# Kernel tuning notes

Measured on AMD Instinct MI355X. Metric: run time of the kernel, lower is better.

The kernel has to match this reference:

```python
import jax, jax.numpy as jnp
import numpy as np

L_MAX = 6
R = 1
IN_IRREPS  = [(256,0),(128,1),(128,2),(64,3),(64,4),(64,5),(64,6)]
HID_IRREPS = [(64,0),(64,1),(64,2),(32,3),(32,4),(32,5),(32,6)]
N_SCALARS = 64
N_GATES = sum(m for m, l in HID_IRREPS if l > 0)  # 256
PRE_IRREPS = [(N_SCALARS,0),(N_GATES,0)] + [(m,l) for m,l in HID_IRREPS if l > 0]
OUT_IRREPS = [(R,l) for l in range(L_MAX+1)]

def _dim(irr):
    return sum(m*(2*l+1) for m, l in irr)

def _wsize(in_irr, out_irr):
    mul_in = {l: m for m, l in in_irr}
    return sum(mul_in[l]*mo for mo, l in out_irr)

def e3linear(x, wflat, in_irr, out_irr):
    # block-diagonal per-irrep linear with e3nn 1/sqrt(fan_in) normalization
    B = x.shape[0]
    blocks = {}
    off = 0
    for mul, l in in_irr:
        d = mul*(2*l+1)
        blocks[l] = (x[:, off:off+d].reshape(B, mul, 2*l+1), mul)
        off += d
    outs = []
    woff = 0
    for mul_out, l in out_irr:
        xb, mul_in = blocks[l]
        w = wflat[woff:woff+mul_in*mul_out].reshape(mul_in, mul_out)
        woff += mul_in*mul_out
        y = jnp.einsum('bim,io->bom', xb, w) * (1.0/np.sqrt(mul_in))
        outs.append(y.reshape(B, mul_out*(2*l+1)))
    return jnp.concatenate(outs, axis=1)

def gate(z):
    # z = [scalars 64x0e | gates 256x0e | gated l>0 irreps]
    s = jax.nn.silu(z[:, :N_SCALARS])
    g = jax.nn.sigmoid(z[:, N_SCALARS:N_SCALARS+N_GATES])
    x = z[:, N_SCALARS+N_GATES:]
    outs = [s]
    goff = 0
    xoff = 0
    for mul, l in HID_IRREPS:
        if l == 0:
            continue
        m = 2*l+1
        xb = x[:, xoff:xoff+mul*m].reshape(-1, mul, m)
        outs.append((xb * g[:, goff:goff+mul, None]).reshape(-1, mul*m))
        goff += mul
        xoff += mul*m
    return jnp.concatenate(outs, axis=1)

def _forward(v_raw, w1, w2, w3, w4):
    x = gate(e3linear(v_raw, w1, IN_IRREPS, PRE_IRREPS))
    x = gate(e3linear(x, w2, HID_IRREPS, PRE_IRREPS))
    x = gate(e3linear(x, w3, HID_IRREPS, PRE_IRREPS))
    c = e3linear(x, w4, HID_IRREPS, OUT_IRREPS)  # [B, 49]
    B = c.shape[0]
    segs = []
    off = 0
    for l in range(L_MAX+1):
        m = 2*l+1
        seg = c[:, off:off+R*m].reshape(B, R, m).transpose(0, 2, 1)  # (B, m, R)
        segs.append(seg)
        off += R*m
    return jnp.concatenate(segs, axis=1)  # (B, 49, R)

def setup_inputs():
    key = jax.random.key(0)
    ks = jax.random.split(key, 5)
    B = 16384
    return {
        "v_raw": jax.random.normal(ks[0], (B, _dim(IN_IRREPS)), jnp.float32),
        "w1": jax.random.normal(ks[1], (_wsize(IN_IRREPS, PRE_IRREPS),), jnp.float32),
        "w2": jax.random.normal(ks[2], (_wsize(HID_IRREPS, PRE_IRREPS),), jnp.float32),
        "w3": jax.random.normal(ks[3], (_wsize(HID_IRREPS, PRE_IRREPS),), jnp.float32),
        "w4": jax.random.normal(ks[4], (_wsize(HID_IRREPS, OUT_IRREPS),), jnp.float32),
    }

def reference(v_raw, w1, w2, w3, w4):
    return _forward(v_raw, w1, w2, w3, w4)
```

## Files before the change

### kernel.cpp

```cpp
#include <hip/hip_runtime.h>
#include <cstddef>


typedef _Float16 half8 __attribute__((ext_vector_type(8)));
typedef float    f32x4 __attribute__((ext_vector_type(4)));
typedef float    fvec4 __attribute__((ext_vector_type(4)));

#define B_ROWS  8
#define IN_DIM  3840
#define OUT_COLS 49

#define OFF_STG0 0
#define OFF_STG1 8064
#define OFF_H0   16128
#define OFF_H1   20608
#define OFF_G1   25088
#define OFF_G2   27200
#define OFF_G3   29312
#define SMEM_ELTS 31424

#define P2BASE 106496
#define P3BASE 139264

__global__ __launch_bounds__(256) void prep_weights(
    const float* __restrict__ w1, const float* __restrict__ w2,
    const float* __restrict__ w3, _Float16* __restrict__ packed)
{
  const int g = blockIdx.x * 256 + threadIdx.x;
  const int K_[24]    = {256,256,128,128,64,64,64,64,  64,64,64,64,32,32,32,32,
                         64,64,64,64,32,32,32,32};
  const int N_[24]    = {64,256,64,64,32,32,32,32,  64,256,64,64,32,32,32,32,
                         64,256,64,64,32,32,32,32};
  const int woff_[24] = {0,16384,81920,90112,98304,100352,102400,104448,
                         0,4096,20480,24576,28672,29696,30720,31744,
                         0,4096,20480,24576,28672,29696,30720,31744};
  const int poff_[24] = {0,16384,81920,90112,98304,100352,102400,104448,
                         106496,110592,126976,131072,135168,136192,137216,138240,
                         139264,143360,159744,163840,167936,168960,169984,171008};
  int bi = 0;
  for (int i = 1; i < 24; ++i) if (g * 8 >= poff_[i]) bi = i;
  const float* w = (bi < 8) ? w1 : ((bi < 16) ? w2 : w3);
  const int rel8 = g - poff_[bi] / 8;
  const int lane = rel8 & 63;
  const int fi   = rel8 >> 6;
  const int K = K_[bi], N = N_[bi];
  const int KF = K >> 5;
  const int kf = fi % KF;
  const int nt = fi / KF;
  const int k0 = kf * 32 + (lane >> 4) * 8;
  const int n  = nt * 16 + (lane & 15);
  const float scale = 1.0f / sqrtf((float)K);
  half8 vv;
#pragma unroll
  for (int j = 0; j < 8; ++j)
    vv[j] = (_Float16)(w[woff_[bi] + (size_t)(k0 + j) * N + n] * scale);
  *(half8*)(packed + (size_t)g * 8) = vv;
}

template<int TWOL1, int MUL>
__device__ __forceinline__ void issue_loads(const float* __restrict__ vraw,
                                            int b0, int inoff, fvec4 (&regs)[7])
{
  constexpr int D  = MUL * TWOL1;
  constexpr int D4 = D / 4;
  constexpr int V4 = D4 * B_ROWS;
  constexpr int NV = (V4 + 255) / 256;
  const int t = threadIdx.x;
#pragma unroll
  for (int v = 0; v < NV; ++v) {
    const int gv = v * 256 + t;
    if ((V4 & 255) == 0 || gv < V4) {
      const int b  = gv / D4;
      const int dd = (gv - b * D4) * 4;
      regs[v] = *(const fvec4*)(vraw + (size_t)(b0 + b) * IN_DIM + inoff + dd);
    }
  }
}

template<int TWOL1, int MUL>
__device__ __forceinline__ void write_stage(const fvec4 (&regs)[7], _Float16* stg)
{
  constexpr int D  = MUL * TWOL1;
  constexpr int D4 = D / 4;
  constexpr int V4 = D4 * B_ROWS;
  constexpr int NV = (V4 + 255) / 256;
  constexpr int KP = MUL + 8;
  const int t = threadIdx.x;
#pragma unroll
  for (int v = 0; v < NV; ++v) {
    const int gv = v * 256 + t;
    if ((V4 & 255) == 0 || gv < V4) {
      const int b  = gv / D4;
      const int dd = (gv - b * D4) * 4;
      const fvec4 x = regs[v];
#pragma unroll
      for (int j = 0; j < 4; ++j) {
        const int d = dd + j;
        const int i = d / TWOL1;
        const int m = d - i * TWOL1;
        stg[(b * TWOL1 + m) * KP + i] = (_Float16)x[j];
      }
    }
  }
}

template<int TWOL1, int K, int N>
__device__ __forceinline__ void gemm_gated(
    const _Float16* __restrict__ A, const _Float16* __restrict__ Bp,
    _Float16* __restrict__ H, const _Float16* __restrict__ G, int goff)
{
  constexpr int R  = 8 * TWOL1;
  constexpr int MT = (R + 15) / 16;
  constexpr int NT = N / 16;
  constexpr int KF = K / 32;
  constexpr int AP = K + 8;
  constexpr int HP = N + 8;
  const int lane = threadIdx.x & 63;
  const int wave = threadIdx.x >> 6;
  const int col  = lane & 15;
  const int quad = lane >> 4;
  for (int t = wave; t < MT * NT; t += 4) {
    const int mt = t % MT;
    const int nt = t / MT;
    f32x4 acc = {0.f, 0.f, 0.f, 0.f};
    const _Float16* ap = A + (mt * 16 + col) * AP + quad * 8;
    const _Float16* bp = Bp + ((size_t)(nt * KF * 64 + lane)) * 8;
#pragma unroll
    for (int kf = 0; kf < KF; ++kf) {
      const half8 av = *(const half8*)(ap + kf * 32);
      const half8 bv = *(const half8*)(bp + kf * 512);
      acc = __builtin_amdgcn_mfma_f32_16x16x32_f16(av, bv, acc, 0, 0, 0);
    }
    const int o = nt * 16 + col;
#pragma unroll
    for (int r = 0; r < 4; ++r) {
      const int row = mt * 16 + quad * 4 + r;
      if (row < R) {
        const int b = row / TWOL1;
        const float gg = (float)G[b * 264 + goff + o];
        H[row * HP + o] = (_Float16)(acc[r] * gg);
      }
    }
  }
}

template<int K>
__device__ __forceinline__ void gemm_scal(
    const _Float16* __restrict__ A, const _Float16* __restrict__ Bs,
    const _Float16* __restrict__ Bg, _Float16* __restrict__ Hs,
    _Float16* __restrict__ Gout)
{
  constexpr int KF = K / 32;
  constexpr int AP = K + 8;
  const int lane = threadIdx.x & 63;
  const int wave = threadIdx.x >> 6;
  const int col  = lane & 15;
  const int quad = lane >> 4;
  const _Float16* ap0 = A + col * AP + quad * 8;
  {
    const int nt = wave;
    f32x4 acc = {0.f, 0.f, 0.f, 0.f};
    const _Float16* bp = Bs + ((size_t)(nt * KF * 64 + lane)) * 8;
#pragma unroll
    for (int kf = 0; kf < KF; ++kf)
      acc = __builtin_amdgcn_mfma_f32_16x16x32_f16(
          *(const half8*)(ap0 + kf * 32), *(const half8*)(bp + kf * 512), acc, 0, 0, 0);
    const int o = nt * 16 + col;
#pragma unroll
    for (int r = 0; r < 4; ++r) {
      const int row = quad * 4 + r;
      if (row < B_ROWS) {
        const float z  = acc[r];
        const float sg = 1.f / (1.f + __expf(-z));
        Hs[row * 72 + o] = (_Float16)(z * sg);
      }
    }
  }
  for (int nt = wave; nt < 16; nt += 4) {
    f32x4 acc = {0.f, 0.f, 0.f, 0.f};
    const _Float16* bp = Bg + ((size_t)(nt * KF * 64 + lane)) * 8;
#pragma unroll
    for (int kf = 0; kf < KF; ++kf)
      acc = __builtin_amdgcn_mfma_f32_16x16x32_f16(
          *(const half8*)(ap0 + kf * 32), *(const half8*)(bp + kf * 512), acc, 0, 0, 0);
    const int o = nt * 16 + col;
#pragma unroll
    for (int r = 0; r < 4; ++r) {
      const int row = quad * 4 + r;
      if (row < B_ROWS)
        Gout[row * 264 + o] = (_Float16)(1.f / (1.f + __expf(-acc[r])));
    }
  }
}

template<int TWOL1, int K>
__device__ __forceinline__ void layer4(
    const _Float16* __restrict__ H, const float* __restrict__ w4, int w4off,
    float* __restrict__ out, int b0, int lsq)
{
  constexpr int R  = 8 * TWOL1;
  constexpr int HP = K + 8;
  const int r = threadIdx.x;
  if (r < R) {
    float s = 0.f;
#pragma unroll
    for (int i = 0; i < K; ++i) s += (float)H[r * HP + i] * w4[w4off + i];
    constexpr float scale = (K == 64) ? 0.125f : 0.17677669529663687f;
    const int b = r / TWOL1;
    const int m = r - b * TWOL1;
    out[(size_t)(b0 + b) * OUT_COLS + lsq + m] = s * scale;
  }
}

__device__ __forceinline__ void compute_chain0(
    const _Float16* stg, _Float16* H0, _Float16* H1,
    _Float16* G1, _Float16* G2, _Float16* G3,
    const _Float16* packed, const float* w4, float* out, int b0)
{
  gemm_scal<256>(stg, packed + 0,          packed + 16384,        H0, G1);
  __syncthreads();
  gemm_scal<64>(H0,  packed + P2BASE + 0,  packed + P2BASE + 4096, H1, G2);
  __syncthreads();
  gemm_scal<64>(H1,  packed + P3BASE + 0,  packed + P3BASE + 4096, H0, G3);
  __syncthreads();
  layer4<1, 64>(H0, w4, 0, out, b0, 0);
}

template<int L>
__device__ __forceinline__ void compute_chain(
    const _Float16* stg, _Float16* H0, _Float16* H1,
    const _Float16* G1, const _Float16* G2, const _Float16* G3,
    const _Float16* packed, const float* w4, float* out, int b0)
{
  constexpr int TWOL1 = 2 * L + 1;
  constexpr int K1 = (L <= 2) ? 128 : 64;
  constexpr int N1 = (L <= 2) ? 64 : 32;
  constexpr int P1OFF[7] = {0, 81920, 90112, 98304, 100352, 102400, 104448};
  constexpr int P2REL[7] = {0, 20480, 24576, 28672, 29696, 30720, 31744};
  constexpr int GOFF[7]  = {0, 0, 64, 128, 160, 192, 224};
  constexpr int W4OFF[7] = {0, 64, 128, 192, 224, 256, 288};
  gemm_gated<TWOL1, K1, N1>(stg, packed + P1OFF[L],          H0, G1, GOFF[L]);
  __syncthreads();
  gemm_gated<TWOL1, N1, N1>(H0,  packed + P2BASE + P2REL[L], H1, G2, GOFF[L]);
  __syncthreads();
  gemm_gated<TWOL1, N1, N1>(H1,  packed + P3BASE + P2REL[L], H0, G3, GOFF[L]);
  __syncthreads();
  layer4<TWOL1, N1>(H0, w4, W4OFF[L], out, b0, L * L);
}

__global__ __launch_bounds__(256) void fused_decoder(
    const float* __restrict__ vraw, const float* __restrict__ w4,
    const _Float16* __restrict__ packed, float* __restrict__ out)
{
  __shared__ __align__(16) _Float16 smem[SMEM_ELTS];
  _Float16* stg0 = smem + OFF_STG0;
  _Float16* stg1 = smem + OFF_STG1;
  _Float16* H0   = smem + OFF_H0;
  _Float16* H1   = smem + OFF_H1;
  _Float16* G1   = smem + OFF_G1;
  _Float16* G2   = smem + OFF_G2;
  _Float16* G3   = smem + OFF_G3;
  const int b0 = blockIdx.x * B_ROWS;
  fvec4 rA[7], rB[7];

  issue_loads<1, 256>(vraw, b0, 0, rA);
  issue_loads<3, 128>(vraw, b0, 256, rB);
  write_stage<1, 256>(rA, stg0);
  __syncthreads();
  compute_chain0(stg0, H0, H1, G1, G2, G3, packed, w4, out, b0);

  write_stage<3, 128>(rB, stg1);
  issue_loads<5, 128>(vraw, b0, 640, rA);
  __syncthreads();
  compute_chain<1>(stg1, H0, H1, G1, G2, G3, packed, w4, out, b0);

  write_stage<5, 128>(rA, stg0);
  issue_loads<7, 64>(vraw, b0, 1280, rB);
  __syncthreads();
  compute_chain<2>(stg0, H0, H1, G1, G2, G3, packed, w4, out, b0);

  write_stage<7, 64>(rB, stg1);
  issue_loads<9, 64>(vraw, b0, 1728, rA);
  __syncthreads();
  compute_chain<3>(stg1, H0, H1, G1, G2, G3, packed, w4, out, b0);

  write_stage<9, 64>(rA, stg0);
  issue_loads<11, 64>(vraw, b0, 2304, rB);
  __syncthreads();
  compute_chain<4>(stg0, H0, H1, G1, G2, G3, packed, w4, out, b0);

  write_stage<11, 64>(rB, stg1);
  issue_loads<13, 64>(vraw, b0, 3008, rA);
  __syncthreads();
  compute_chain<5>(stg1, H0, H1, G1, G2, G3, packed, w4, out, b0);

  write_stage<13, 64>(rA, stg0);
  __syncthreads();
  compute_chain<6>(stg0, H0, H1, G1, G2, G3, packed, w4, out, b0);
}

extern "C" void kernel_launch(void* const* d_in, const int* in_sizes, int n_in,
                              void* d_out, int out_size, void* d_ws, size_t ws_size,
                              hipStream_t stream)
{
  (void)in_sizes; (void)n_in; (void)out_size; (void)ws_size;
  const float* vraw = (const float*)d_in[0];
  const float* w1   = (const float*)d_in[1];
  const float* w2   = (const float*)d_in[2];
  const float* w3   = (const float*)d_in[3];
  const float* w4   = (const float*)d_in[4];
  float* out = (float*)d_out;
  _Float16* packed = (_Float16*)d_ws;

  prep_weights<<<84, 256, 0, stream>>>(w1, w2, w3, packed);
  fused_decoder<<<16384 / B_ROWS, 256, 0, stream>>>(vraw, w4, packed, out);
}
```

Before: 445.5 us.

## Swap MFMA operand roles, single staging buffer, interleave irrep chains to cut barriers

Weights now serve as the MFMA A operand and activations as B, so each lane's accumulator holds four consecutive output channels. Gated outputs, gate reads and sigmoid results are then written with half4 vector LDS accesses. The staging buffers collapse to one, and each irrep's first-layer GEMM is folded into the previous chain's tail, which removes some barriers and cuts LDS use. Launch bounds now request 3 blocks per SM, and layer4 reads half8 vectors. The risks are more register pressure from the occupancy hint and a tighter reuse schedule for the shared staging buffer.

```diff
diff --git a/kernel.cpp b/kernel.cpp
--- a/kernel.cpp
+++ b/kernel.cpp
@@ -3,21 +3,23 @@
 
 
 typedef _Float16 half8 __attribute__((ext_vector_type(8)));
+typedef _Float16 half4 __attribute__((ext_vector_type(4)));
 typedef float    f32x4 __attribute__((ext_vector_type(4)));
 typedef float    fvec4 __attribute__((ext_vector_type(4)));
 
-#define B_ROWS  8
-#define IN_DIM  3840
+#define B_ROWS   8
+#define IN_DIM   3840
 #define OUT_COLS 49
 
-#define OFF_STG0 0
-#define OFF_STG1 8064
-#define OFF_H0   16128
-#define OFF_H1   20608
-#define OFF_G1   25088
-#define OFF_G2   27200
-#define OFF_G3   29312
-#define SMEM_ELTS 31424
+#define OFF_STG  0
+#define OFF_HA   8064
+#define OFF_HB   12544
+#define OFF_HSA  17024
+#define OFF_HSB  18176
+#define OFF_G1   19328
+#define OFF_G2   21440
+#define OFF_G3   23552
+#define SMEM_ELTS 25664
 
 #define P2BASE 106496
 #define P3BASE 139264
@@ -26,18 +28,19 @@
     const float* __restrict__ w1, const float* __restrict__ w2,
     const float* __restrict__ w3, _Float16* __restrict__ packed)
 {
+  static const int K_[24]    = {256,256,128,128,64,64,64,64,  64,64,64,64,32,32,32,32,
+                                64,64,64,64,32,32,32,32};
+  static const int N_[24]    = {64,256,64,64,32,32,32,32,  64,256,64,64,32,32,32,32,
+                                64,256,64,64,32,32,32,32};
+  static const int woff_[24] = {0,16384,81920,90112,98304,100352,102400,104448,
+                                0,4096,20480,24576,28672,29696,30720,31744,
+                                0,4096,20480,24576,28672,29696,30720,31744};
+  static const int poff_[24] = {0,16384,81920,90112,98304,100352,102400,104448,
+                                106496,110592,126976,131072,135168,136192,137216,138240,
+                                139264,143360,159744,163840,167936,168960,169984,171008};
   const int g = blockIdx.x * 256 + threadIdx.x;
-  const int K_[24]    = {256,256,128,128,64,64,64,64,  64,64,64,64,32,32,32,32,
-                         64,64,64,64,32,32,32,32};
-  const int N_[24]    = {64,256,64,64,32,32,32,32,  64,256,64,64,32,32,32,32,
-                         64,256,64,64,32,32,32,32};
-  const int woff_[24] = {0,16384,81920,90112,98304,100352,102400,104448,
-                         0,4096,20480,24576,28672,29696,30720,31744,
-                         0,4096,20480,24576,28672,29696,30720,31744};
-  const int poff_[24] = {0,16384,81920,90112,98304,100352,102400,104448,
-                         106496,110592,126976,131072,135168,136192,137216,138240,
-                         139264,143360,159744,163840,167936,168960,169984,171008};
   int bi = 0;
+#pragma unroll
   for (int i = 1; i < 24; ++i) if (g * 8 >= poff_[i]) bi = i;
   const float* w = (bi < 8) ? w1 : ((bi < 16) ? w2 : w3);
   const int rel8 = g - poff_[bi] / 8;
@@ -46,14 +49,14 @@
   const int K = K_[bi], N = N_[bi];
   const int KF = K >> 5;
   const int kf = fi % KF;
-  const int nt = fi / KF;
+  const int mt = fi / KF;
   const int k0 = kf * 32 + (lane >> 4) * 8;
-  const int n  = nt * 16 + (lane & 15);
+  const int o  = mt * 16 + (lane & 15);
   const float scale = 1.0f / sqrtf((float)K);
   half8 vv;
 #pragma unroll
   for (int j = 0; j < 8; ++j)
-    vv[j] = (_Float16)(w[woff_[bi] + (size_t)(k0 + j) * N + n] * scale);
+    vv[j] = (_Float16)(w[woff_[bi] + (size_t)(k0 + j) * N + o] * scale);
   *(half8*)(packed + (size_t)g * 8) = vv;
 }
 
@@ -104,14 +107,30 @@
   }
 }
 
+__device__ __forceinline__ void ws_l0(const fvec4 (&regs)[7], _Float16* stg)
+{
+  const int t = threadIdx.x;
+#pragma unroll
+  for (int v = 0; v < 2; ++v) {
+    const int gv = v * 256 + t;
+    const int b  = gv >> 6;
+    const int i0 = (gv & 63) * 4;
+    const fvec4 x = regs[v];
+    half4 h;
+#pragma unroll
+    for (int j = 0; j < 4; ++j) h[j] = (_Float16)x[j];
+    *(half4*)(stg + b * 264 + i0) = h;
+  }
+}
+
 template<int TWOL1, int K, int N>
-__device__ __forceinline__ void gemm_gated(
-    const _Float16* __restrict__ A, const _Float16* __restrict__ Bp,
+__device__ __forceinline__ void gemm_sw(
+    const _Float16* __restrict__ Bact, const _Float16* __restrict__ Ap,
     _Float16* __restrict__ H, const _Float16* __restrict__ G, int goff)
 {
   constexpr int R  = 8 * TWOL1;
-  constexpr int MT = (R + 15) / 16;
-  constexpr int NT = N / 16;
+  constexpr int NT = (R + 15) / 16;
+  constexpr int MT = N / 16;
   constexpr int KF = K / 32;
   constexpr int AP = K + 8;
   constexpr int HP = N + 8;
@@ -123,31 +142,31 @@
     const int mt = t % MT;
     const int nt = t / MT;
     f32x4 acc = {0.f, 0.f, 0.f, 0.f};
-    const _Float16* ap = A + (mt * 16 + col) * AP + quad * 8;
-    const _Float16* bp = Bp + ((size_t)(nt * KF * 64 + lane)) * 8;
+    const _Float16* bp = Bact + (nt * 16 + col) * AP + quad * 8;
+    const _Float16* ap = Ap + ((size_t)(mt * KF * 64 + lane)) * 8;
 #pragma unroll
     for (int kf = 0; kf < KF; ++kf) {
-      const half8 av = *(const half8*)(ap + kf * 32);
-      const half8 bv = *(const half8*)(bp + kf * 512);
+      const half8 av = *(const half8*)(ap + kf * 512);
+      const half8 bv = *(const half8*)(bp + kf * 32);
       acc = __builtin_amdgcn_mfma_f32_16x16x32_f16(av, bv, acc, 0, 0, 0);
     }
-    const int o = nt * 16 + col;
-#pragma unroll
-    for (int r = 0; r < 4; ++r) {
-      const int row = mt * 16 + quad * 4 + r;
-      if (row < R) {
-        const int b = row / TWOL1;
-        const float gg = (float)G[b * 264 + goff + o];
-        H[row * HP + o] = (_Float16)(acc[r] * gg);
-      }
+    const int c = nt * 16 + col;
+    if (c < R) {
+      const int b  = c / TWOL1;
+      const int o0 = mt * 16 + quad * 4;
+      const half4 g4 = *(const half4*)(G + b * 264 + goff + o0);
+      half4 hv;
+#pragma unroll
+      for (int r = 0; r < 4; ++r) hv[r] = (_Float16)(acc[r] * (float)g4[r]);
+      *(half4*)(H + c * HP + o0) = hv;
     }
   }
 }
 
 template<int K>
-__device__ __forceinline__ void gemm_scal(
-    const _Float16* __restrict__ A, const _Float16* __restrict__ Bs,
-    const _Float16* __restrict__ Bg, _Float16* __restrict__ Hs,
+__device__ __forceinline__ void scal_sw(
+    const _Float16* __restrict__ Bact, const _Float16* __restrict__ ApS,
+    const _Float16* __restrict__ ApG, _Float16* __restrict__ HsOut,
     _Float16* __restrict__ Gout)
 {
   constexpr int KF = K / 32;
@@ -156,45 +175,46 @@
   const int wave = threadIdx.x >> 6;
   const int col  = lane & 15;
   const int quad = lane >> 4;
-  const _Float16* ap0 = A + col * AP + quad * 8;
+  const _Float16* bp = Bact + col * AP + quad * 8;
   {
-    const int nt = wave;
+    const int mt = wave;
     f32x4 acc = {0.f, 0.f, 0.f, 0.f};
-    const _Float16* bp = Bs + ((size_t)(nt * KF * 64 + lane)) * 8;
+    const _Float16* ap = ApS + ((size_t)(mt * KF * 64 + lane)) * 8;
 #pragma unroll
     for (int kf = 0; kf < KF; ++kf)
       acc = __builtin_amdgcn_mfma_f32_16x16x32_f16(
-          *(const half8*)(ap0 + kf * 32), *(const half8*)(bp + kf * 512), acc, 0, 0, 0);
-    const int o = nt * 16 + col;
-#pragma unroll
-    for (int r = 0; r < 4; ++r) {
-      const int row = quad * 4 + r;
-      if (row < B_ROWS) {
-        const float z  = acc[r];
-        const float sg = 1.f / (1.f + __expf(-z));
-        Hs[row * 72 + o] = (_Float16)(z * sg);
+          *(const half8*)(ap + kf * 512), *(const half8*)(bp + kf * 32), acc, 0, 0, 0);
+    if (col < B_ROWS) {
+      const int o0 = mt * 16 + quad * 4;
+      half4 hv;
+#pragma unroll
+      for (int r = 0; r < 4; ++r) {
+        const float z = acc[r];
+        hv[r] = (_Float16)(z * __builtin_amdgcn_rcpf(1.f + __expf(-z)));
       }
-    }
-  }
-  for (int nt = wave; nt < 16; nt += 4) {
+      *(half4*)(HsOut + col * 72 + o0) = hv;
+    }
+  }
+  for (int mt = wave; mt < 16; mt += 4) {
     f32x4 acc = {0.f, 0.f, 0.f, 0.f};
-    const _Float16* bp = Bg + ((size_t)(nt * KF * 64 + lane)) * 8;
+    const _Float16* ap = ApG + ((size_t)(mt * KF * 64 + lane)) * 8;
 #pragma unroll
     for (int kf = 0; kf < KF; ++kf)
       acc = __builtin_amdgcn_mfma_f32_16x16x32_f16(
-          *(const half8*)(ap0 + kf * 32), *(const half8*)(bp + kf * 512), acc, 0, 0, 0);
-    const int o = nt * 16 + col;
-#pragma unroll
-    for (int r = 0; r < 4; ++r) {
-      const int row = quad * 4 + r;
-      if (row < B_ROWS)
-        Gout[row * 264 + o] = (_Float16)(1.f / (1.f + __expf(-acc[r])));
+          *(const half8*)(ap + kf * 512), *(const half8*)(bp + kf * 32), acc, 0, 0, 0);
+    if (col < B_ROWS) {
+      const int o0 = mt * 16 + quad * 4;
+      half4 gv;
+#pragma unroll
+      for (int r = 0; r < 4; ++r)
+        gv[r] = (_Float16)__builtin_amdgcn_rcpf(1.f + __expf(-acc[r]));
+      *(half4*)(Gout + col * 264 + o0) = gv;
     }
   }
 }
 
 template<int TWOL1, int K>
-__device__ __forceinline__ void layer4(
+__device__ __forceinline__ void layer4_sw(
     const _Float16* __restrict__ H, const float* __restrict__ w4, int w4off,
     float* __restrict__ out, int b0, int lsq)
 {
@@ -204,99 +224,97 @@
   if (r < R) {
     float s = 0.f;
 #pragma unroll
-    for (int i = 0; i < K; ++i) s += (float)H[r * HP + i] * w4[w4off + i];
+    for (int i8 = 0; i8 < K / 8; ++i8) {
+      const half8 hv = *(const half8*)(H + r * HP + i8 * 8);
+#pragma unroll
+      for (int j = 0; j < 8; ++j) s += (float)hv[j] * w4[w4off + i8 * 8 + j];
+    }
     constexpr float scale = (K == 64) ? 0.125f : 0.17677669529663687f;
-    const int b = r / TWOL1;
-    const int m = r - b * TWOL1;
-    out[(size_t)(b0 + b) * OUT_COLS + lsq + m] = s * scale;
-  }
-}
-
-__device__ __forceinline__ void compute_chain0(
-    const _Float16* stg, _Float16* H0, _Float16* H1,
-    _Float16* G1, _Float16* G2, _Float16* G3,
-    const _Float16* packed, const float* w4, float* out, int b0)
-{
-  gemm_scal<256>(stg, packed + 0,          packed + 16384,        H0, G1);
-  __syncthreads();
-  gemm_scal<64>(H0,  packed + P2BASE + 0,  packed + P2BASE + 4096, H1, G2);
-  __syncthreads();
-  gemm_scal<64>(H1,  packed + P3BASE + 0,  packed + P3BASE + 4096, H0, G3);
-  __syncthreads();
-  layer4<1, 64>(H0, w4, 0, out, b0, 0);
-}
-
-template<int L>
-__device__ __forceinline__ void compute_chain(
-    const _Float16* stg, _Float16* H0, _Float16* H1,
-    const _Float16* G1, const _Float16* G2, const _Float16* G3,
-    const _Float16* packed, const float* w4, float* out, int b0)
-{
-  constexpr int TWOL1 = 2 * L + 1;
-  constexpr int K1 = (L <= 2) ? 128 : 64;
-  constexpr int N1 = (L <= 2) ? 64 : 32;
-  constexpr int P1OFF[7] = {0, 81920, 90112, 98304, 100352, 102400, 104448};
-  constexpr int P2REL[7] = {0, 20480, 24576, 28672, 29696, 30720, 31744};
-  constexpr int GOFF[7]  = {0, 0, 64, 128, 160, 192, 224};
-  constexpr int W4OFF[7] = {0, 64, 128, 192, 224, 256, 288};
-  gemm_gated<TWOL1, K1, N1>(stg, packed + P1OFF[L],          H0, G1, GOFF[L]);
-  __syncthreads();
-  gemm_gated<TWOL1, N1, N1>(H0,  packed + P2BASE + P2REL[L], H1, G2, GOFF[L]);
-  __syncthreads();
-  gemm_gated<TWOL1, N1, N1>(H1,  packed + P3BASE + P2REL[L], H0, G3, GOFF[L]);
-  __syncthreads();
-  layer4<TWOL1, N1>(H0, w4, W4OFF[L], out, b0, L * L);
-}
-
-__global__ __launch_bounds__(256) void fused_decoder(
+    out[(size_t)(b0 + r / TWOL1) * OUT_COLS + lsq + (r % TWOL1)] = s * scale;
+  }
+}
+
+__global__ __launch_bounds__(256, 3) void fused_decoder(
     const float* __restrict__ vraw, const float* __restrict__ w4,
     const _Float16* __restrict__ packed, float* __restrict__ out)
 {
   __shared__ __align__(16) _Float16 smem[SMEM_ELTS];
-  _Float16* stg0 = smem + OFF_STG0;
-  _Float16* stg1 = smem + OFF_STG1;
-  _Float16* H0   = smem + OFF_H0;
-  _Float16* H1   = smem + OFF_H1;
-  _Float16* G1   = smem + OFF_G1;
-  _Float16* G2   = smem + OFF_G2;
-  _Float16* G3   = smem + OFF_G3;
+  _Float16* STG = smem + OFF_STG;
+  _Float16* HA  = smem + OFF_HA;
+  _Float16* HB  = smem + OFF_HB;
+  _Float16* HsA = smem + OFF_HSA;
+  _Float16* HsB = smem + OFF_HSB;
+  _Float16* G1  = smem + OFF_G1;
+  _Float16* G2  = smem + OFF_G2;
+  _Float16* G3  = smem + OFF_G3;
   const int b0 = blockIdx.x * B_ROWS;
+  const _Float16* pk = packed;
   fvec4 rA[7], rB[7];
 
   issue_loads<1, 256>(vraw, b0, 0, rA);
   issue_loads<3, 128>(vraw, b0, 256, rB);
-  write_stage<1, 256>(rA, stg0);
-  __syncthreads();
-  compute_chain0(stg0, H0, H1, G1, G2, G3, packed, w4, out, b0);
-
-  write_stage<3, 128>(rB, stg1);
+  ws_l0(rA, STG);
+  __syncthreads();
+  scal_sw<256>(STG, pk + 0, pk + 16384, HsA, G1);
+  __syncthreads();
+  write_stage<3, 128>(rB, STG);
   issue_loads<5, 128>(vraw, b0, 640, rA);
-  __syncthreads();
-  compute_chain<1>(stg1, H0, H1, G1, G2, G3, packed, w4, out, b0);
-
-  write_stage<5, 128>(rA, stg0);
+  scal_sw<64>(HsA, pk + P2BASE, pk + P2BASE + 4096, HsB, G2);
+  __syncthreads();
+  scal_sw<64>(HsB, pk + P3BASE, pk + P3BASE + 4096, HsA, G3);
+  __syncthreads();
+  layer4_sw<1, 64>(HsA, w4, 0, out, b0, 0);
+  gemm_sw<3, 128, 64>(STG, pk + 81920, HA, G1, 0);
+  __syncthreads();
+  write_stage<5, 128>(rA, STG);
   issue_loads<7, 64>(vraw, b0, 1280, rB);
-  __syncthreads();
-  compute_chain<2>(stg0, H0, H1, G1, G2, G3, packed, w4, out, b0);
-
-  write_stage<7, 64>(rB, stg1);
+  gemm_sw<3, 64, 64>(HA, pk + P2BASE + 20480, HB, G2, 0);
+  __syncthreads();
+  gemm_sw<3, 64, 64>(HB, pk + P3BASE + 20480, HA, G3, 0);
+  __syncthreads();
+  layer4_sw<3, 64>(HA, w4, 64, out, b0, 1);
+  gemm_sw<5, 128, 64>(STG, pk + 90112, HB, G1, 64);
+  __syncthreads();
+  write_stage<7, 64>(rB, STG);
   issue_loads<9, 64>(vraw, b0, 1728, rA);
-  __syncthreads();
-  compute_chain<3>(stg1, H0, H1, G1, G2, G3, packed, w4, out, b0);
-
-  write_stage<9, 64>(rA, stg0);
+  gemm_sw<5, 64, 64>(HB, pk + P2BASE + 24576, HA, G2, 64);
+  __syncthreads();
+  gemm_sw<5, 64, 64>(HA, pk + P3BASE + 24576, HB, G3, 64);
+  __syncthreads();
+  layer4_sw<5, 64>(HB, w4, 128, out, b0, 4);
+  gemm_sw<7, 64, 32>(STG, pk + 98304, HA, G1, 128);
+  __syncthreads();
+  write_stage<9, 64>(rA, STG);
   issue_loads<11, 64>(vraw, b0, 2304, rB);
-  __syncthreads();
-  compute_chain<4>(stg0, H0, H1, G1, G2, G3, packed, w4, out, b0);
-
-  write_stage<11, 64>(rB, stg1);
+  gemm_sw<7, 32, 32>(HA, pk + P2BASE + 28672, HB, G2, 128);
+  __syncthreads();
+  gemm_sw<7, 32, 32>(HB, pk + P3BASE + 28672, HA, G3, 128);
+  __syncthreads();
+  layer4_sw<7, 32>(HA, w4, 192, out, b0, 9);
+  gemm_sw<9, 64, 32>(STG, pk + 100352, HB, G1, 160);
+  __syncthreads();
+  write_stage<11, 64>(rB, STG);
   issue_loads<13, 64>(vraw, b0, 3008, rA);
-  __syncthreads();
-  compute_chain<5>(stg1, H0, H1, G1, G2, G3, packed, w4, out, b0);
-
-  write_stage<13, 64>(rA, stg0);
-  __syncthreads();
-  compute_chain<6>(stg0, H0, H1, G1, G2, G3, packed, w4, out, b0);
+  gemm_sw<9, 32, 32>(HB, pk + P2BASE + 29696, HA, G2, 160);
+  __syncthreads();
+  gemm_sw<9, 32, 32>(HA, pk + P3BASE + 29696, HB, G3, 160);
+  __syncthreads();
+  layer4_sw<9, 32>(HB, w4, 224, out, b0, 16);
+  gemm_sw<11, 64, 32>(STG, pk + 102400, HA, G1, 192);
+  __syncthreads();
+  write_stage<13, 64>(rA, STG);
+  gemm_sw<11, 32, 32>(HA, pk + P2BASE + 30720, HB, G2, 192);
+  __syncthreads();
+  gemm_sw<11, 32, 32>(HB, pk + P3BASE + 30720, HA, G3, 192);
+  __syncthreads();
+  layer4_sw<11, 32>(HA, w4, 256, out, b0, 25);
+  gemm_sw<13, 64, 32>(STG, pk + 104448, HB, G1, 224);
+  __syncthreads();
+  gemm_sw<13, 32, 32>(HB, pk + P2BASE + 31744, HA, G2, 224);
+  __syncthreads();
+  gemm_sw<13, 32, 32>(HA, pk + P3BASE + 31744, HB, G3, 224);
+  __syncthreads();
+  layer4_sw<13, 32>(HB, w4, 288, out, b0, 36);
 }
 
 extern "C" void kernel_launch(void* const* d_in, const int* in_sizes, int n_in,
```

Result: faster. 391.1 us (-12.2%).
